# Performance work log

Hardware: AMD Instinct MI355X
Metric: run time of the kernel (lower is better)

The kernel has to match this reference:

```python
import jax, jax.numpy as jnp
import numpy as np

L, B, N, D, H = 4, 4, 2048, 512, 8
HD = D // H  # head dim 64
EPS = 1e-5

def setup_inputs() -> dict:
    key = jax.random.key(0)
    ks = jax.random.split(key, 8)
    s = 0.02  # init scale for weights
    f32 = jnp.float32
    return {
        "x": jax.random.normal(ks[0], (B, N, D), f32),
        "Wq": jax.random.normal(ks[1], (L, D, D), f32) * s,
        "Wk": jax.random.normal(ks[2], (L, D, D), f32) * s,
        "Wv": jax.random.normal(ks[3], (L, D, D), f32) * s,
        "Wo": jax.random.normal(ks[4], (L, D, D), f32) * s,
        "bo": jnp.zeros((L, D), f32),
        "ln1_g": jnp.ones((L, D), f32),
        "ln1_b": jnp.zeros((L, D), f32),
        "W1": jax.random.normal(ks[5], (L, D, D), f32) * s,
        "b1": jnp.zeros((L, D), f32),
        "W2": jax.random.normal(ks[6], (L, D, D), f32) * s,
        "b2": jnp.zeros((L, D), f32),
        "ln2_g": jnp.ones((L, D), f32),
        "ln2_b": jnp.zeros((L, D), f32),
    }

def _layernorm(x, g, b):
    mu = jnp.mean(x, axis=-1, keepdims=True)
    var = jnp.mean(jnp.square(x - mu), axis=-1, keepdims=True)
    return (x - mu) * jax.lax.rsqrt(var + EPS) * g + b

def reference(x, Wq, Wk, Wv, Wo, bo, ln1_g, ln1_b, W1, b1, W2, b2, ln2_g, ln2_b):
    scale = D ** -0.5  # dim1 == dim on the cfg=None path

    def layer(h, p):
        wq, wk, wv, wo, bo_, g1, bb1, w1, bh1, w2, bh2, g2, bb2 = p
        # --- Residual(PreNorm(Attention)) ---
        y = _layernorm(h, g1, bb1)
        def split_heads(t):  # [B,N,D] -> [B,H,N,HD]
            return t.reshape(B, N, H, HD).transpose(0, 2, 1, 3)
        q = split_heads(y @ wq)
        k = split_heads(y @ wk)
        v = split_heads(y @ wv)
        dots = jnp.einsum('bhid,bhjd->bhij', q, k) * scale
        attn = jax.nn.softmax(dots, axis=-1)
        o = jnp.einsum('bhij,bhjd->bhid', attn, v)
        o = o.transpose(0, 2, 1, 3).reshape(B, N, D)
        h = h + o @ wo + bo_
        # --- Residual(PreNorm(FeedForward)) ---
        y = _layernorm(h, g2, bb2)
        y = jax.nn.gelu(y @ w1 + bh1, approximate=False)
        h = h + y @ w2 + bh2
        return h, None

    params = (Wq, Wk, Wv, Wo, bo, ln1_g, ln1_b, W1, b1, W2, b2, ln2_g, ln2_b)
    out, _ = jax.lax.scan(layer, x, params)
    return out
```

## Files before the change

kernel.cpp:

```cpp
#include <hip/hip_runtime.h>
#include <hip/hip_bf16.h>


typedef __bf16 bf16x8 __attribute__((ext_vector_type(8)));
typedef short short4v __attribute__((ext_vector_type(4)));
typedef float f32x4 __attribute__((ext_vector_type(4)));
typedef unsigned int u32x4 __attribute__((ext_vector_type(4)));
typedef unsigned int u32x2 __attribute__((ext_vector_type(2)));
typedef unsigned short u16;

__device__ __forceinline__ u16 f2b(float f) {
  unsigned int u; __builtin_memcpy(&u, &f, 4);
  u += 0x7fffu + ((u >> 16) & 1u);
  return (u16)(u >> 16);
}
__device__ __forceinline__ bf16x8 ld8(const u16* p) {
  u32x4 t = *(const u32x4*)p;
  bf16x8 r; __builtin_memcpy(&r, &t, 16); return r;
}
__device__ __forceinline__ short4v ld4(const u16* p) {
  u32x2 t = *(const u32x2*)p;
  short4v r; __builtin_memcpy(&r, &t, 8); return r;
}
__device__ __forceinline__ unsigned pkhi(float a, float b) {
  unsigned ua, ub; __builtin_memcpy(&ua, &a, 4); __builtin_memcpy(&ub, &b, 4);
  return __builtin_amdgcn_perm(ua, ub, 0x07060302u);
}

#define GLL(gp, lp) __builtin_amdgcn_global_load_lds( \
    (const __attribute__((address_space(1))) void*)(gp), \
    (__attribute__((address_space(3))) void*)(lp), 16, 0, 0)

__device__ __forceinline__ int swz(int r) { return (r + (r >> 2)) & 3; }

__global__ __launch_bounds__(256) void tr_all_k(
    const float* __restrict__ Wq, const float* __restrict__ Wk,
    const float* __restrict__ Wv, const float* __restrict__ Wo,
    const float* __restrict__ W1, const float* __restrict__ W2,
    u16* __restrict__ wtqkv, u16* __restrict__ wto,
    u16* __restrict__ wt1, u16* __restrict__ wt2) {
  __shared__ float t[32][33];
  int tx = threadIdx.x, ty = threadIdx.y;
  int z = blockIdx.z, which = z >> 2, l = z & 3;
  const float* in;
  u16* out;
  switch (which) {
    case 0: in = Wq; out = wtqkv + l * 786432; break;
    case 1: in = Wk; out = wtqkv + l * 786432 + 262144; break;
    case 2: in = Wv; out = wtqkv + l * 786432 + 524288; break;
    case 3: in = Wo; out = wto + l * 262144; break;
    case 4: in = W1; out = wt1 + l * 262144; break;
    default: in = W2; out = wt2 + l * 262144; break;
  }
  int k0 = blockIdx.y * 32, n0 = blockIdx.x * 32;
  const float* ip = in + l * 262144;
#pragma unroll
  for (int i = 0; i < 4; i++)
    t[ty + i * 8][tx] = ip[(k0 + ty + i * 8) * 512 + n0 + tx];
  __syncthreads();
#pragma unroll
  for (int i = 0; i < 4; i++)
    out[(n0 + ty + i * 8) * 512 + k0 + tx] = f2b(t[tx][ty + i * 8]);
}

__global__ __launch_bounds__(256) void ln_k(const float* __restrict__ h,
                                            const float* __restrict__ gg,
                                            const float* __restrict__ bb,
                                            u16* __restrict__ y) {
  int tid = threadIdx.x, wave = tid >> 6, lane = tid & 63;
  int tok = blockIdx.x * 4 + wave;
  const float* hp = h + (size_t)tok * 512 + lane * 8;
  float x[8];
  *(float4*)&x[0] = *(const float4*)hp;
  *(float4*)&x[4] = *(const float4*)(hp + 4);
  float s = 0.f, ss = 0.f;
#pragma unroll
  for (int i = 0; i < 8; i++) { s += x[i]; ss += x[i] * x[i]; }
#pragma unroll
  for (int off = 1; off < 64; off <<= 1) {
    s += __shfl_xor(s, off, 64);
    ss += __shfl_xor(ss, off, 64);
  }
  float mean = s * (1.0f / 512.0f);
  float var = ss * (1.0f / 512.0f) - mean * mean;
  float rstd = rsqrtf(var + 1e-5f);
  u32x4 ov;
#pragma unroll
  for (int i = 0; i < 4; i++) {
    int d0 = lane * 8 + i * 2;
    float y0 = (x[i * 2]     - mean) * rstd * gg[d0]     + bb[d0];
    float y1 = (x[i * 2 + 1] - mean) * rstd * gg[d0 + 1] + bb[d0 + 1];
    ov[i] = (unsigned)f2b(y0) | ((unsigned)f2b(y1) << 16);
  }
  *(u32x4*)&y[(size_t)tok * 512 + lane * 8] = ov;
}

enum { EPI_RES = 1, EPI_GELU = 2 };

template <int EPI>
__global__ __launch_bounds__(256, 4) void gemm2_k(
    const u16* __restrict__ A, const u16* __restrict__ Bt,
    const float* __restrict__ bias, u16* __restrict__ out0,
    const float* __restrict__ hin, float* __restrict__ hout,
    float* __restrict__ fout) {
  __shared__ __align__(16) u16 As[2][64 * 32];
  __shared__ __align__(16) u16 Bs[2][128 * 32];
  const int tid = threadIdx.x;
  const int wave = tid >> 6, lane = tid & 63;
  const int quad = lane >> 4, l16 = lane & 15;
  const int wm = wave >> 1, wn = wave & 1;
  const int m0 = blockIdx.x * 64;
  const int n0 = blockIdx.y * 128;
  const int mb = m0 + wm * 32, nb = n0 + wn * 64;

  float hr[2][4][4];
  if constexpr (EPI == EPI_RES) {
#pragma unroll
    for (int mi = 0; mi < 2; ++mi)
#pragma unroll
      for (int ni = 0; ni < 4; ++ni) {
        int r0 = mb + mi * 16 + quad * 4, c = nb + ni * 16 + l16;
#pragma unroll
        for (int g = 0; g < 4; ++g)
          hr[mi][ni][g] = hin[(size_t)(r0 + g) * 512 + c];
      }
  }

  f32x4 acc[2][4];
#pragma unroll
  for (int i = 0; i < 2; i++)
#pragma unroll
    for (int j = 0; j < 4; j++) acc[i][j] = f32x4{0.f, 0.f, 0.f, 0.f};

  const int sA0 = wave * 64 + lane;
  const int rowA = sA0 >> 2, cgA = (sA0 & 3) ^ swz(rowA);
  const size_t agl = (size_t)(m0 + rowA) * 512 + cgA * 8;
  int rowB[2], cgB[2];
#pragma unroll
  for (int rnd = 0; rnd < 2; ++rnd) {
    int s = rnd * 256 + sA0;
    rowB[rnd] = s >> 2;
    cgB[rnd] = (s & 3) ^ swz(rowB[rnd]);
  }
  const size_t bgl0 = (size_t)(n0 + rowB[0]) * 512 + cgB[0] * 8;
  const size_t bgl1 = (size_t)(n0 + rowB[1]) * 512 + cgB[1] * 8;

  int kbA[2], kbB[4];
#pragma unroll
  for (int mi = 0; mi < 2; ++mi) {
    int r = wm * 32 + mi * 16 + l16;
    kbA[mi] = r * 32 + (quad ^ swz(r)) * 8;
  }
#pragma unroll
  for (int ni = 0; ni < 4; ++ni) {
    int r = wn * 64 + ni * 16 + l16;
    kbB[ni] = r * 32 + (quad ^ swz(r)) * 8;
  }

  GLL(A + agl, &As[0][(wave * 64) * 8]);
  GLL(Bt + bgl0, &Bs[0][(wave * 64) * 8]);
  GLL(Bt + bgl1, &Bs[0][(256 + wave * 64) * 8]);

#pragma unroll 2
  for (int kt = 0; kt < 16; ++kt) {
    __syncthreads();
    const u16* AsB = As[kt & 1];
    const u16* BsB = Bs[kt & 1];
    if (kt + 1 < 16) {
      u16* AsN = (u16*)As[(kt & 1) ^ 1];
      u16* BsN = (u16*)Bs[(kt & 1) ^ 1];
      const int k1 = (kt + 1) * 32;
      GLL(A + agl + k1, AsN + (wave * 64) * 8);
      GLL(Bt + bgl0 + k1, BsN + (wave * 64) * 8);
      GLL(Bt + bgl1 + k1, BsN + (256 + wave * 64) * 8);
    }

    bf16x8 af[2], bf_[4];
#pragma unroll
    for (int mi = 0; mi < 2; ++mi) af[mi] = ld8(AsB + kbA[mi]);
#pragma unroll
    for (int ni = 0; ni < 4; ++ni) bf_[ni] = ld8(BsB + kbB[ni]);
#pragma unroll
    for (int mi = 0; mi < 2; ++mi)
#pragma unroll
      for (int ni = 0; ni < 4; ++ni)
        acc[mi][ni] = __builtin_amdgcn_mfma_f32_16x16x32_bf16(
            af[mi], bf_[ni], acc[mi][ni], 0, 0, 0);
  }

#pragma unroll
  for (int mi = 0; mi < 2; ++mi) {
#pragma unroll
    for (int ni = 0; ni < 4; ++ni) {
      f32x4 a = acc[mi][ni];
      int r0 = mb + mi * 16 + quad * 4;
      int c = nb + ni * 16 + l16;
      float bi = bias[c];
      if constexpr (EPI == EPI_RES) {
#pragma unroll
        for (int g = 0; g < 4; ++g) {
          float v = hr[mi][ni][g] + a[g] + bi;
          hout[(size_t)(r0 + g) * 512 + c] = v;
          if (fout) fout[(size_t)(r0 + g) * 512 + c] = v;
        }
      } else {
#pragma unroll
        for (int g = 0; g < 4; ++g) {
          float t = a[g] + bi;
          float gl = 0.5f * t * (1.0f + erff(t * 0.70710678118654752f));
          out0[(size_t)(r0 + g) * 512 + c] = f2b(gl);
        }
      }
    }
  }
}

__global__ __launch_bounds__(256, 4) void gemm_qkv_k(
    const u16* __restrict__ A, const u16* __restrict__ Bt,
    u16* __restrict__ outq, u16* __restrict__ outk, u16* __restrict__ outvt) {
  __shared__ __align__(16) u16 As[128 * 32];
  __shared__ __align__(16) u16 Bs[128 * 32];
  const int tid = threadIdx.x;
  const int wave = tid >> 6, lane = tid & 63;
  const int quad = lane >> 4, l16 = lane & 15;
  const int wm = wave >> 1, wn = wave & 1;
  const int m0 = blockIdx.x * 128;
  const int n0 = blockIdx.y * 128;

  f32x4 acc[4][4];
#pragma unroll
  for (int i = 0; i < 4; i++)
#pragma unroll
    for (int j = 0; j < 4; j++) acc[i][j] = f32x4{0.f, 0.f, 0.f, 0.f};

  const int sA0 = wave * 64 + lane;

  for (int kt = 0; kt < 16; ++kt) {
    const int k0 = kt * 32;
    __syncthreads();
#pragma unroll
    for (int rnd = 0; rnd < 2; ++rnd) {
      int s = rnd * 256 + sA0;
      int row = s >> 2, c = s & 3;
      int cg = c ^ swz(row);
      GLL(A + (size_t)(m0 + row) * 512 + k0 + cg * 8, &As[(rnd * 256 + wave * 64) * 8]);
      GLL(Bt + (size_t)(n0 + row) * 512 + k0 + cg * 8, &Bs[(rnd * 256 + wave * 64) * 8]);
    }
    __syncthreads();

    bf16x8 af[4], bf_[4];
#pragma unroll
    for (int mi = 0; mi < 4; ++mi) {
      int r = wm * 64 + mi * 16 + l16;
      af[mi] = ld8(&As[r * 32 + (quad ^ swz(r)) * 8]);
    }
#pragma unroll
    for (int ni = 0; ni < 4; ++ni) {
      int r = wn * 64 + ni * 16 + l16;
      bf_[ni] = ld8(&Bs[r * 32 + (quad ^ swz(r)) * 8]);
    }
#pragma unroll
    for (int mi = 0; mi < 4; ++mi)
#pragma unroll
      for (int ni = 0; ni < 4; ++ni)
        acc[mi][ni] = __builtin_amdgcn_mfma_f32_16x16x32_bf16(
            af[mi], bf_[ni], acc[mi][ni], 0, 0, 0);
  }

  const int mb = m0 + wm * 64, nb = n0 + wn * 64;
#pragma unroll
  for (int mi = 0; mi < 4; ++mi) {
#pragma unroll
    for (int ni = 0; ni < 4; ++ni) {
      f32x4 a = acc[mi][ni];
      int r0 = mb + mi * 16 + quad * 4;
      int c = nb + ni * 16 + l16;
      if (c < 512) {
        const float C2 = 0.06375871506958306f;
#pragma unroll
        for (int g = 0; g < 4; ++g) outq[(size_t)(r0 + g) * 512 + c] = f2b(a[g] * C2);
      } else if (c < 1024) {
#pragma unroll
        for (int g = 0; g < 4; ++g) outk[(size_t)(r0 + g) * 512 + (c - 512)] = f2b(a[g]);
      } else {
        int cv = c - 1024, hh = cv >> 6, dd = cv & 63;
        int bb = r0 >> 11, nt = r0 & 2047;
        u32x2 pk;
        pk[0] = (unsigned)f2b(a[0]) | ((unsigned)f2b(a[1]) << 16);
        pk[1] = (unsigned)f2b(a[2]) | ((unsigned)f2b(a[3]) << 16);
        *(u32x2*)&outvt[((size_t)(bb * 8 + hh) * 64 + dd) * 2048 + nt] = pk;
      }
    }
  }
}

__global__ __launch_bounds__(256, 4) void attn_k(const u16* __restrict__ q,
                                                 const u16* __restrict__ k,
                                                 const u16* __restrict__ vt,
                                                 u16* __restrict__ o) {
  __shared__ __align__(16) u16 Ks[2][64 * 64];
  __shared__ __align__(16) u16 Vs[2][64 * 64];
  __shared__ float Lr[4][32];
  const int tid = threadIdx.x, wave = tid >> 6, lane = tid & 63;
  const int quad = lane >> 4, l16 = lane & 15;
  const int qh = quad >> 1, ql = quad & 1;
  const int swl = l16 & 7;
  const int qh2 = wave & 1, kvs = wave >> 1;
  const int bh = blockIdx.x, b = bh >> 3, h = bh & 7;
  const int qt0 = blockIdx.y * 64;

  const u16* qpb = q + (size_t)(b * 2048 + qt0 + qh2 * 32) * 512 + h * 64;
  bf16x8 aq[2][2];
#pragma unroll
  for (int qt = 0; qt < 2; ++qt) {
    const u16* qp = qpb + (size_t)(qt * 16 + l16) * 512;
    aq[qt][0] = ld8(qp + quad * 8);
    aq[qt][1] = ld8(qp + 32 + quad * 8);
  }

  const u16* kp = k + (size_t)b * 2048 * 512 + h * 64;
  const u16* vp = vt + (size_t)bh * 64 * 2048;

  const int srow = lane >> 3, schk = lane & 7, sgc = schk ^ srow;
  const int krow0 = wave * 8 + srow;
  const size_t kgl0 = (size_t)krow0 * 512 + sgc * 8;
  const size_t kgl1 = (size_t)(krow0 + 32) * 512 + sgc * 8;
  const size_t vgl0 = (size_t)krow0 * 2048 + sgc * 8;
  const size_t vgl1 = (size_t)(krow0 + 32) * 2048 + sgc * 8;

  int kb[2][2];
#pragma unroll
  for (int t = 0; t < 2; ++t) {
    kb[t][0] = (kvs * 32 + t * 16 + l16) * 64 + ((quad)     ^ swl) * 8;
    kb[t][1] = (kvs * 32 + t * 16 + l16) * 64 + ((4 + quad) ^ swl) * 8;
  }
  int vb[2];
#pragma unroll
  for (int t = 0; t < 2; ++t)
    vb[t] = l16 * 64 + ((kvs * 4 + t * 2 + qh) ^ swl) * 8 + ql * 4;

  f32x4 oacc[4][2];
#pragma unroll
  for (int i = 0; i < 4; i++)
#pragma unroll
    for (int j = 0; j < 2; j++) oacc[i][j] = f32x4{0.f, 0.f, 0.f, 0.f};
  float ls[2] = {0.f, 0.f};

  GLL(kp + kgl0, &Ks[0][(wave * 8) * 64]);
  GLL(kp + kgl1, &Ks[0][(32 + wave * 8) * 64]);
  GLL(vp + vgl0, &Vs[0][(wave * 8) * 64]);
  GLL(vp + vgl1, &Vs[0][(32 + wave * 8) * 64]);

#pragma unroll 2
  for (int kt = 0; kt < 32; ++kt) {
    __syncthreads();
    const u16* KsB = Ks[kt & 1];
    const u16* VsB = Vs[kt & 1];
    if (kt + 1 < 32) {
      u16* KsN = (u16*)Ks[(kt & 1) ^ 1];
      u16* VsN = (u16*)Vs[(kt & 1) ^ 1];
      const u16* kpn = kp + (size_t)(kt + 1) * 32768;
      const u16* vpn = vp + (size_t)(kt + 1) * 64;
      GLL(kpn + kgl0, KsN + (wave * 8) * 64);
      GLL(kpn + kgl1, KsN + (32 + wave * 8) * 64);
      GLL(vpn + vgl0, VsN + (wave * 8) * 64);
      GLL(vpn + vgl1, VsN + (32 + wave * 8) * 64);
    }

    short4v pp[2][2];
#pragma unroll
    for (int t = 0; t < 2; ++t) {
      bf16x8 kf0 = ld8(KsB + kb[t][0]);
      bf16x8 kf1 = ld8(KsB + kb[t][1]);
#pragma unroll
      for (int qt = 0; qt < 2; ++qt) {
        f32x4 sa = f32x4{0.f, 0.f, 0.f, 0.f};
        sa = __builtin_amdgcn_mfma_f32_16x16x32_bf16(kf0, aq[qt][0], sa, 0, 0, 0);
        sa = __builtin_amdgcn_mfma_f32_16x16x32_bf16(kf1, aq[qt][1], sa, 0, 0, 0);
        float p0 = __builtin_amdgcn_exp2f(sa[0]);
        float p1 = __builtin_amdgcn_exp2f(sa[1]);
        float p2 = __builtin_amdgcn_exp2f(sa[2]);
        float p3 = __builtin_amdgcn_exp2f(sa[3]);
        ls[qt] += (p0 + p1) + (p2 + p3);
        u32x2 pk; pk[0] = pkhi(p1, p0); pk[1] = pkhi(p3, p2);
        __builtin_memcpy(&pp[t][qt], &pk, 8);
      }
    }

#pragma unroll
    for (int dt = 0; dt < 4; ++dt)
#pragma unroll
      for (int t = 0; t < 2; ++t) {
        short4v av = ld4(VsB + vb[t] + dt * 1024);
#pragma unroll
        for (int qt = 0; qt < 2; ++qt)
          oacc[dt][qt] = __builtin_amdgcn_mfma_f32_16x16x16bf16_1k(
              av, pp[t][qt], oacc[dt][qt], 0, 0, 0);
      }
  }

#pragma unroll
  for (int qt = 0; qt < 2; ++qt) {
    ls[qt] += __shfl_xor(ls[qt], 16, 64);
    ls[qt] += __shfl_xor(ls[qt], 32, 64);
  }
  if (quad == 0) {
#pragma unroll
    for (int qt = 0; qt < 2; ++qt) Lr[wave][qt * 16 + l16] = ls[qt];
  }
  __syncthreads();

  float* R = (float*)&Ks[0][0];
  const int l7 = lane & 7;
  if (wave >= 2) {
    float* Rw = R + (wave - 2) * 2048;
#pragma unroll
    for (int dt = 0; dt < 4; ++dt)
#pragma unroll
      for (int qt = 0; qt < 2; ++qt) {
        int s = (dt * 2 + qt) ^ l7;
        *(f32x4*)&Rw[lane * 32 + s * 4] = oacc[dt][qt];
      }
  }
  __syncthreads();
  if (wave < 2) {
    float* Rw = R + wave * 2048;
    float inv[2];
#pragma unroll
    for (int qt = 0; qt < 2; ++qt)
      inv[qt] = 1.0f / (Lr[wave][qt * 16 + l16] + Lr[wave + 2][qt * 16 + l16]);
#pragma unroll
    for (int dt = 0; dt < 4; ++dt)
#pragma unroll
      for (int qt = 0; qt < 2; ++qt) {
        int s = (dt * 2 + qt) ^ l7;
        f32x4 v = *(f32x4*)&Rw[lane * 32 + s * 4];
        float i4 = inv[qt];
        float o0 = (oacc[dt][qt][0] + v[0]) * i4;
        float o1 = (oacc[dt][qt][1] + v[1]) * i4;
        float o2 = (oacc[dt][qt][2] + v[2]) * i4;
        float o3 = (oacc[dt][qt][3] + v[3]) * i4;
        u16* op = o + (size_t)(b * 2048 + qt0 + wave * 32 + qt * 16 + l16) * 512 +
                  h * 64 + dt * 16 + quad * 4;
        u32x2 pk;
        pk[0] = (unsigned)f2b(o0) | ((unsigned)f2b(o1) << 16);
        pk[1] = (unsigned)f2b(o2) | ((unsigned)f2b(o3) << 16);
        *(u32x2*)op = pk;
      }
  }
}

extern "C" void kernel_launch(void* const* d_in, const int* in_sizes, int n_in,
                              void* d_out, int out_size, void* d_ws,
                              size_t ws_size, hipStream_t stream) {
  const float* x   = (const float*)d_in[0];
  const float* Wq  = (const float*)d_in[1];
  const float* Wk  = (const float*)d_in[2];
  const float* Wv  = (const float*)d_in[3];
  const float* Wo  = (const float*)d_in[4];
  const float* bo  = (const float*)d_in[5];
  const float* g1  = (const float*)d_in[6];
  const float* bg1 = (const float*)d_in[7];
  const float* W1  = (const float*)d_in[8];
  const float* b1  = (const float*)d_in[9];
  const float* W2  = (const float*)d_in[10];
  const float* b2  = (const float*)d_in[11];
  const float* g2  = (const float*)d_in[12];
  const float* bg2 = (const float*)d_in[13];

  char* ws = (char*)d_ws;
  float* h    = (float*)ws;
  u16* yb     = (u16*)(ws + (16ll << 20));
  u16* qb     = (u16*)(ws + (24ll << 20));
  u16* kb     = (u16*)(ws + (32ll << 20));
  u16* vtb    = (u16*)(ws + (40ll << 20));
  u16* ob     = (u16*)(ws + (48ll << 20));
  u16* wtqkv  = (u16*)(ws + (56ll << 20));
  u16* wto    = (u16*)(ws + (62ll << 20));
  u16* wt1    = (u16*)(ws + (64ll << 20));
  u16* wt2    = (u16*)(ws + (66ll << 20));

  tr_all_k<<<dim3(16, 16, 24), dim3(32, 8), 0, stream>>>(
      Wq, Wk, Wv, Wo, W1, W2, wtqkv, wto, wt1, wt2);

  for (int l = 0; l < 4; ++l) {
    const float* hsrc = (l == 0) ? x : h;
    ln_k<<<2048, 256, 0, stream>>>(hsrc, g1 + l * 512, bg1 + l * 512, yb);
    gemm_qkv_k<<<dim3(64, 12), 256, 0, stream>>>(
        yb, wtqkv + l * 786432, qb, kb, vtb);
    attn_k<<<dim3(32, 32), 256, 0, stream>>>(qb, kb, vtb, ob);
    gemm2_k<EPI_RES><<<dim3(128, 4), 256, 0, stream>>>(
        ob, wto + l * 262144, bo + l * 512, nullptr, hsrc, h, nullptr);
    ln_k<<<2048, 256, 0, stream>>>(h, g2 + l * 512, bg2 + l * 512, yb);
    gemm2_k<EPI_GELU><<<dim3(128, 4), 256, 0, stream>>>(
        yb, wt1 + l * 262144, b1 + l * 512, qb, nullptr, nullptr, nullptr);
    gemm2_k<EPI_RES><<<dim3(128, 4), 256, 0, stream>>>(
        qb, wt2 + l * 262144, b2 + l * 512, nullptr, h, h,
        (l == 3) ? (float*)d_out : nullptr);
  }
}
```

Measured before the change: 581.0 us.

## Double-buffer QKV GEMM LDS tiles and merge PV MFMAs into 16x16x32

The QKV projection GEMM now uses two LDS buffers, prefetching the next K-tile with global_load_lds while the current one feeds the MFMAs. This replaces the two barriers per iteration with one and hoists the address math out of the loop. In attention, the P·V product now packs two 16-wide key chunks into one 16x16x32 bf16 MFMA instead of two 16x16x16 ones, and s_setprio is placed around the MFMA bursts. The cost is double the LDS in the GEMM, which may reduce occupancy, plus the risk that the changed P/V fragment ordering does not match between operands.

```diff
diff --git a/kernel.cpp b/kernel.cpp
--- a/kernel.cpp
+++ b/kernel.cpp
@@ -3,7 +3,6 @@
 
 
 typedef __bf16 bf16x8 __attribute__((ext_vector_type(8)));
-typedef short short4v __attribute__((ext_vector_type(4)));
 typedef float f32x4 __attribute__((ext_vector_type(4)));
 typedef unsigned int u32x4 __attribute__((ext_vector_type(4)));
 typedef unsigned int u32x2 __attribute__((ext_vector_type(2)));
@@ -17,10 +16,6 @@
 __device__ __forceinline__ bf16x8 ld8(const u16* p) {
   u32x4 t = *(const u32x4*)p;
   bf16x8 r; __builtin_memcpy(&r, &t, 16); return r;
-}
-__device__ __forceinline__ short4v ld4(const u16* p) {
-  u32x2 t = *(const u32x2*)p;
-  short4v r; __builtin_memcpy(&r, &t, 8); return r;
 }
 __device__ __forceinline__ unsigned pkhi(float a, float b) {
   unsigned ua, ub; __builtin_memcpy(&ua, &a, 4); __builtin_memcpy(&ub, &b, 4);
@@ -218,8 +213,8 @@
 __global__ __launch_bounds__(256, 4) void gemm_qkv_k(
     const u16* __restrict__ A, const u16* __restrict__ Bt,
     u16* __restrict__ outq, u16* __restrict__ outk, u16* __restrict__ outvt) {
-  __shared__ __align__(16) u16 As[128 * 32];
-  __shared__ __align__(16) u16 Bs[128 * 32];
+  __shared__ __align__(16) u16 As[2][128 * 32];
+  __shared__ __align__(16) u16 Bs[2][128 * 32];
   const int tid = threadIdx.x;
   const int wave = tid >> 6, lane = tid & 63;
   const int quad = lane >> 4, l16 = lane & 15;
@@ -234,31 +229,52 @@
     for (int j = 0; j < 4; j++) acc[i][j] = f32x4{0.f, 0.f, 0.f, 0.f};
 
   const int sA0 = wave * 64 + lane;
-
+  size_t agl[2], bgl[2];
+#pragma unroll
+  for (int rnd = 0; rnd < 2; ++rnd) {
+    int s = rnd * 256 + sA0;
+    int row = s >> 2, cg = (s & 3) ^ swz(row);
+    agl[rnd] = (size_t)(m0 + row) * 512 + cg * 8;
+    bgl[rnd] = (size_t)(n0 + row) * 512 + cg * 8;
+  }
+
+  int kbA[4], kbB[4];
+#pragma unroll
+  for (int mi = 0; mi < 4; ++mi) {
+    int r = wm * 64 + mi * 16 + l16;
+    kbA[mi] = r * 32 + (quad ^ swz(r)) * 8;
+  }
+#pragma unroll
+  for (int ni = 0; ni < 4; ++ni) {
+    int r = wn * 64 + ni * 16 + l16;
+    kbB[ni] = r * 32 + (quad ^ swz(r)) * 8;
+  }
+
+  GLL(A + agl[0], &As[0][(wave * 64) * 8]);
+  GLL(A + agl[1], &As[0][(256 + wave * 64) * 8]);
+  GLL(Bt + bgl[0], &Bs[0][(wave * 64) * 8]);
+  GLL(Bt + bgl[1], &Bs[0][(256 + wave * 64) * 8]);
+
+#pragma unroll 2
   for (int kt = 0; kt < 16; ++kt) {
-    const int k0 = kt * 32;
     __syncthreads();
-#pragma unroll
-    for (int rnd = 0; rnd < 2; ++rnd) {
-      int s = rnd * 256 + sA0;
-      int row = s >> 2, c = s & 3;
-      int cg = c ^ swz(row);
-      GLL(A + (size_t)(m0 + row) * 512 + k0 + cg * 8, &As[(rnd * 256 + wave * 64) * 8]);
-      GLL(Bt + (size_t)(n0 + row) * 512 + k0 + cg * 8, &Bs[(rnd * 256 + wave * 64) * 8]);
-    }
-    __syncthreads();
+    const u16* AsB = As[kt & 1];
+    const u16* BsB = Bs[kt & 1];
+    if (kt + 1 < 16) {
+      u16* AsN = (u16*)As[(kt & 1) ^ 1];
+      u16* BsN = (u16*)Bs[(kt & 1) ^ 1];
+      const int k1 = (kt + 1) * 32;
+      GLL(A + agl[0] + k1, AsN + (wave * 64) * 8);
+      GLL(A + agl[1] + k1, AsN + (256 + wave * 64) * 8);
+      GLL(Bt + bgl[0] + k1, BsN + (wave * 64) * 8);
+      GLL(Bt + bgl[1] + k1, BsN + (256 + wave * 64) * 8);
+    }
 
     bf16x8 af[4], bf_[4];
 #pragma unroll
-    for (int mi = 0; mi < 4; ++mi) {
-      int r = wm * 64 + mi * 16 + l16;
-      af[mi] = ld8(&As[r * 32 + (quad ^ swz(r)) * 8]);
-    }
-#pragma unroll
-    for (int ni = 0; ni < 4; ++ni) {
-      int r = wn * 64 + ni * 16 + l16;
-      bf_[ni] = ld8(&Bs[r * 32 + (quad ^ swz(r)) * 8]);
-    }
+    for (int mi = 0; mi < 4; ++mi) af[mi] = ld8(AsB + kbA[mi]);
+#pragma unroll
+    for (int ni = 0; ni < 4; ++ni) bf_[ni] = ld8(BsB + kbB[ni]);
 #pragma unroll
     for (int mi = 0; mi < 4; ++mi)
 #pragma unroll
@@ -303,7 +319,6 @@
   __shared__ float Lr[4][32];
   const int tid = threadIdx.x, wave = tid >> 6, lane = tid & 63;
   const int quad = lane >> 4, l16 = lane & 15;
-  const int qh = quad >> 1, ql = quad & 1;
   const int swl = l16 & 7;
   const int qh2 = wave & 1, kvs = wave >> 1;
   const int bh = blockIdx.x, b = bh >> 3, h = bh & 7;
@@ -334,10 +349,8 @@
     kb[t][0] = (kvs * 32 + t * 16 + l16) * 64 + ((quad)     ^ swl) * 8;
     kb[t][1] = (kvs * 32 + t * 16 + l16) * 64 + ((4 + quad) ^ swl) * 8;
   }
-  int vb[2];
-#pragma unroll
-  for (int t = 0; t < 2; ++t)
-    vb[t] = l16 * 64 + ((kvs * 4 + t * 2 + qh) ^ swl) * 8 + ql * 4;
+  const int vblo = l16 * 64 + (((kvs << 2) + (quad >> 1)) ^ swl) * 8 + (quad & 1) * 4;
+  const int vbhi = l16 * 64 + (((kvs << 2) + 2 + (quad >> 1)) ^ swl) * 8 + (quad & 1) * 4;
 
   f32x4 oacc[4][2];
 #pragma unroll
@@ -367,7 +380,7 @@
       GLL(vpn + vgl1, VsN + (32 + wave * 8) * 64);
     }
 
-    short4v pp[2][2];
+    unsigned pk[2][2][2];
 #pragma unroll
     for (int t = 0; t < 2; ++t) {
       bf16x8 kf0 = ld8(KsB + kb[t][0]);
@@ -375,28 +388,43 @@
 #pragma unroll
       for (int qt = 0; qt < 2; ++qt) {
         f32x4 sa = f32x4{0.f, 0.f, 0.f, 0.f};
+        __builtin_amdgcn_s_setprio(1);
         sa = __builtin_amdgcn_mfma_f32_16x16x32_bf16(kf0, aq[qt][0], sa, 0, 0, 0);
         sa = __builtin_amdgcn_mfma_f32_16x16x32_bf16(kf1, aq[qt][1], sa, 0, 0, 0);
+        __builtin_amdgcn_s_setprio(0);
         float p0 = __builtin_amdgcn_exp2f(sa[0]);
         float p1 = __builtin_amdgcn_exp2f(sa[1]);
         float p2 = __builtin_amdgcn_exp2f(sa[2]);
         float p3 = __builtin_amdgcn_exp2f(sa[3]);
         ls[qt] += (p0 + p1) + (p2 + p3);
-        u32x2 pk; pk[0] = pkhi(p1, p0); pk[1] = pkhi(p3, p2);
-        __builtin_memcpy(&pp[t][qt], &pk, 8);
+        pk[t][qt][0] = pkhi(p1, p0);
+        pk[t][qt][1] = pkhi(p3, p2);
       }
     }
 
-#pragma unroll
-    for (int dt = 0; dt < 4; ++dt)
-#pragma unroll
-      for (int t = 0; t < 2; ++t) {
-        short4v av = ld4(VsB + vb[t] + dt * 1024);
-#pragma unroll
-        for (int qt = 0; qt < 2; ++qt)
-          oacc[dt][qt] = __builtin_amdgcn_mfma_f32_16x16x16bf16_1k(
-              av, pp[t][qt], oacc[dt][qt], 0, 0, 0);
-      }
+    bf16x8 pf[2];
+#pragma unroll
+    for (int qt = 0; qt < 2; ++qt) {
+      u32x4 w;
+      w[0] = pk[0][qt][0]; w[1] = pk[0][qt][1];
+      w[2] = pk[1][qt][0]; w[3] = pk[1][qt][1];
+      __builtin_memcpy(&pf[qt], &w, 16);
+    }
+
+    __builtin_amdgcn_s_setprio(1);
+#pragma unroll
+    for (int dt = 0; dt < 4; ++dt) {
+      u32x2 lo = *(const u32x2*)(VsB + vblo + dt * 1024);
+      u32x2 hi = *(const u32x2*)(VsB + vbhi + dt * 1024);
+      u32x4 w;
+      w[0] = lo[0]; w[1] = lo[1]; w[2] = hi[0]; w[3] = hi[1];
+      bf16x8 av; __builtin_memcpy(&av, &w, 16);
+#pragma unroll
+      for (int qt = 0; qt < 2; ++qt)
+        oacc[dt][qt] = __builtin_amdgcn_mfma_f32_16x16x32_bf16(
+            av, pf[qt], oacc[dt][qt], 0, 0, 0);
+    }
+    __builtin_amdgcn_s_setprio(0);
   }
 
 #pragma unroll
```

After: 574.7 us. Within noise of the previous version (-1.1%).
